# Optimization experiments

Measured on AMD Instinct MI355X. Metric: run time of the kernel, lower is better.

Reference implementation:

```python
import jax, jax.numpy as jnp
import numpy as np


def setup_inputs() -> dict:
    key = jax.random.key(0)
    k1, k2, k3, k4 = jax.random.split(key, 4)
    B, T, F_in, F_out, N, E, K = 16, 64, 64, 64, 128, 2, 4
    x = jax.random.normal(k1, (B, T, F_in, N), dtype=jnp.float32)
    # graph shift operator per (batch, time, edge-feature); scaled to keep powers bounded
    S = jax.random.normal(k2, (B, T, E, N, N), dtype=jnp.float32) / np.sqrt(N)
    H = jax.random.normal(k3, (F_out, E, K, F_in), dtype=jnp.float32) * 0.02
    bias = jax.random.normal(k4, (F_out, 1), dtype=jnp.float32) * 0.02
    return {"x": x, "S": S, "H": H, "bias": bias}


def reference(x, S, H, bias):
    # x: [B,T,F_in,N], S: [B,T,E,N,N], H: [F_out,E,K,F_in], bias: [F_out,1]
    B, T, F_in, N = x.shape
    E = S.shape[2]
    F_out, _, K, _ = H.shape
    # replicate features across edge-feature dim: [B,T,E,F_in,N]
    cur = jnp.broadcast_to(x[:, :, None], (B, T, E, F_in, N))
    taps = [cur]
    zero_row = jnp.zeros((B, 1, E, F_in, N), dtype=x.dtype)
    for _ in range(1, K):
        # time-shift: tap k at time t depends on tap k-1 at time t-1
        cur = jnp.concatenate([zero_row, cur[:, :-1]], axis=1)
        # diffuse over graph: [..,F_in,N] @ [..,N,N]
        cur = jnp.matmul(cur, S)
        taps.append(cur)
    z = jnp.stack(taps, axis=2)  # [B,T,K,E,F_in,N]
    # [B,T,N, E*K*F_in], matching permute(0,1,5,3,2,4) in the source
    z = z.transpose(0, 1, 5, 3, 2, 4).reshape(B, T, N, E * K * F_in)
    Hm = H.reshape(F_out, E * K * F_in)
    y = jnp.einsum('btnf,of->bton', z, Hm)  # [B,T,F_out,N]
    return y + bias  # bias [F_out,1] broadcasts over N
```

## Files before the change

kernel.cpp:

```cpp
#include <hip/hip_runtime.h>


namespace {
constexpr int B = 16, T = 64, F = 64, N = 128, E = 2, K = 4;
constexpr int SSW = 136;
constexpr int SZW = 136;
constexpr int TC = 8;
}

typedef short v8s __attribute__((ext_vector_type(8)));
typedef float v4f __attribute__((ext_vector_type(4)));

__device__ inline ushort f2bf(float f) {
  union { float f; uint u; } v; v.f = f;
  uint u = v.u;
  return (ushort)((u + 0x7fffu + ((u >> 16) & 1u)) >> 16);
}

__device__ inline uint pk2(float a, float b) {
  return (uint)f2bf(a) | ((uint)f2bf(b) << 16);
}

__device__ inline void tr64x128(const float* __restrict__ src,
                                ushort* __restrict__ dst, int dstride,
                                ushort* sh, int tid) {
  float4 r0[4], r1[4];
  #pragma unroll
  for (int it = 0; it < 4; ++it) {
    const int idx = tid + it * 256;
    const int m = idx >> 4, g = idx & 15;
    r0[it] = *(const float4*)(src + m * N + g * 8);
    r1[it] = *(const float4*)(src + m * N + g * 8 + 4);
  }
  #pragma unroll
  for (int it = 0; it < 4; ++it) {
    const int idx = tid + it * 256;
    const int m = idx >> 4, g = idx & 15;
    uint4 wv;
    wv.x = pk2(r0[it].x, r0[it].y); wv.y = pk2(r0[it].z, r0[it].w);
    wv.z = pk2(r1[it].x, r1[it].y); wv.w = pk2(r1[it].z, r1[it].w);
    *(uint4*)&sh[m * SSW + ((g ^ (m >> 3)) * 8)] = wv;
  }
  __syncthreads();
  const int bb = tid & 7, a = (tid >> 3) & 15, hh = tid >> 7;
  v8s rows[8];
  #pragma unroll
  for (int j = 0; j < 8; ++j)
    rows[j] = *(const v8s*)&sh[(8 * bb + j) * SSW + ((a ^ bb) * 8)];
  #pragma unroll
  for (int i = 0; i < 4; ++i) {
    const int e = 4 * hh + i;
    const int n = 8 * a + e;
    uint4 wv;
    wv.x = (uint)(ushort)rows[0][e] | ((uint)(ushort)rows[1][e] << 16);
    wv.y = (uint)(ushort)rows[2][e] | ((uint)(ushort)rows[3][e] << 16);
    wv.z = (uint)(ushort)rows[4][e] | ((uint)(ushort)rows[5][e] << 16);
    wv.w = (uint)(ushort)rows[6][e] | ((uint)(ushort)rows[7][e] << 16);
    *(uint4*)(dst + n * dstride + 8 * bb) = wv;
  }
}

__global__ __launch_bounds__(256) void gf_prep(
    const float* __restrict__ x, const float* __restrict__ H,
    ushort* __restrict__ xT, ushort* __restrict__ Hb) {
  __shared__ ushort sh[64 * SSW];
  const int bid = blockIdx.x;
  const int tid = threadIdx.x;
  if (bid < B * T) {
    tr64x128(x + (size_t)bid * F * N, xT + (size_t)bid * N * F, F, sh, tid);
  } else {
    const int hb = bid - B * T;
    const int d = (hb * 256 + tid) * 4;
    const int f = d & 63, o = (d >> 6) & 63, k = (d >> 12) & 3, e = (d >> 14) & 1;
    const float4 v = *(const float4*)(H + (((size_t)o * E + e) * K + k) * F + f);
    uint2 wv;
    wv.x = pk2(v.x, v.y);
    wv.y = pk2(v.z, v.w);
    *(uint2*)(Hb + d) = wv;
  }
}

__global__ __launch_bounds__(256, 2) void gf_fused(
    const float* __restrict__ S, const ushort* __restrict__ xT,
    const ushort* __restrict__ Hb, const float* __restrict__ bias,
    float* __restrict__ y) {
  __shared__ ushort sS[128 * SSW];
  __shared__ ushort sSt[6][16 * SZW];
  const int g = blockIdx.x;
  const int xcd = g & 7, loc = g >> 3;
  const int os = loc & 3, unitL = loc >> 2;
  const int unit = xcd * 16 + unitL;
  const int b = unit >> 3, chunk = unit & 7;
  const int t0 = chunk * TC;
  const int ob = os * 16;
  const int tid = threadIdx.x, w = tid >> 6, lane = tid & 63;
  const int l15 = lane & 15, q = lane >> 4;

  for (int i = tid; i < 6 * 16 * SZW; i += 256) ((ushort*)sSt)[i] = 0;

  v4f Yac[2];
  Yac[0][0] = 0.f; Yac[0][1] = 0.f; Yac[0][2] = 0.f; Yac[0][3] = 0.f;
  Yac[1] = Yac[0];

  const int tstart = (t0 == 0) ? 0 : t0 - 3;
  const int tS0 = (t0 == 0) ? 0 : t0 - 2;

  float4 pf0[8], pf1[8];
  {
    const float* Sg = S + (size_t)((b * T + tS0) * E + 0) * (N * N);
    #pragma unroll
    for (int j = 0; j < 8; ++j) {
      const int idx = tid + j * 256;
      const int m = idx >> 4, g2 = idx & 15;
      pf0[j] = *(const float4*)(Sg + m * N + g2 * 8);
      pf1[j] = *(const float4*)(Sg + m * N + g2 * 8 + 4);
    }
  }
  __syncthreads();

  for (int t = tstart; t < t0 + TC; ++t) {
    const bool staged = (t >= tS0);
    const bool emit = (t >= t0);
    for (int e = 0; e < E; ++e) {
      if (staged) {
        #pragma unroll
        for (int j = 0; j < 8; ++j) {
          const int idx = tid + j * 256;
          const int m = idx >> 4, g2 = idx & 15;
          uint4 wv;
          wv.x = pk2(pf0[j].x, pf0[j].y); wv.y = pk2(pf0[j].z, pf0[j].w);
          wv.z = pk2(pf1[j].x, pf1[j].y); wv.w = pk2(pf1[j].z, pf1[j].w);
          *(uint4*)&sS[m * SSW + ((g2 ^ (m >> 3)) * 8)] = wv;
        }
        const int nt = (e == 0) ? t : t + 1;
        const int ne = (e == 0) ? 1 : 0;
        if (nt < t0 + TC) {
          const float* Sg = S + (size_t)((b * T + nt) * E + ne) * (N * N);
          #pragma unroll
          for (int j = 0; j < 8; ++j) {
            const int idx = tid + j * 256;
            const int m = idx >> 4, g2 = idx & 15;
            pf0[j] = *(const float4*)(Sg + m * N + g2 * 8);
            pf1[j] = *(const float4*)(Sg + m * N + g2 * 8 + 4);
          }
        }
      }

      v4f Pn[2], Qn[2], U3n[2];
      #pragma unroll
      for (int mt = 0; mt < 2; ++mt) {
        Pn[mt][0] = 0.f; Pn[mt][1] = 0.f; Pn[mt][2] = 0.f; Pn[mt][3] = 0.f;
        Qn[mt] = Pn[mt]; U3n[mt] = Pn[mt];
      }
      {
        const ushort* xrow = xT + (size_t)(b * T + t) * (N * F);
        v8s xf[2][2];
        #pragma unroll
        for (int mt = 0; mt < 2; ++mt)
          #pragma unroll
          for (int fk = 0; fk < 2; ++fk)
            xf[mt][fk] = *(const v8s*)(xrow + ((2 * w + mt) * 16 + l15) * F +
                                       fk * 32 + q * 8);
        #pragma unroll
        for (int k = 0; k < 4; ++k) {
          if (k == 0 && !emit) continue;
          const ushort* hrow = Hb + ((size_t)((e * K + k) * 64) + ob + l15) * 64;
          v8s hf[2];
          hf[0] = *(const v8s*)(hrow + q * 8);
          hf[1] = *(const v8s*)(hrow + 32 + q * 8);
          v4f* tgt = (k == 0) ? Yac : (k == 1 ? Pn : (k == 2 ? Qn : U3n));
          #pragma unroll
          for (int fk = 0; fk < 2; ++fk)
            #pragma unroll
            for (int mt = 0; mt < 2; ++mt)
              tgt[mt] = __builtin_amdgcn_mfma_f32_16x16x32_bf16(
                  xf[mt][fk], hf[fk], tgt[mt], 0, 0, 0);
        }
      }

      if (staged) {
        __syncthreads();
        const int a2 = tid & 15, bg = tid >> 4;
        v8s rows[8];
        #pragma unroll
        for (int j = 0; j < 8; ++j)
          rows[j] = *(const v8s*)&sS[(8 * a2 + j) * SSW + ((bg ^ a2) * 8)];
        __syncthreads();
        #pragma unroll
        for (int i = 0; i < 8; ++i) {
          uint4 wv;
          wv.x = (uint)(ushort)rows[0][i] | ((uint)(ushort)rows[1][i] << 16);
          wv.y = (uint)(ushort)rows[2][i] | ((uint)(ushort)rows[3][i] << 16);
          wv.z = (uint)(ushort)rows[4][i] | ((uint)(ushort)rows[5][i] << 16);
          wv.w = (uint)(ushort)rows[6][i] | ((uint)(ushort)rows[7][i] << 16);
          *(uint4*)&sS[(8 * bg + i) * SSW + ((a2 ^ bg) * 8)] = wv;
        }
        __syncthreads();
        __builtin_amdgcn_s_setprio(1);
        #pragma unroll
        for (int c = 0; c < 4; ++c) {
          const int p = ((4 * c + q) + 2 * l15) & 15;
          const int sbase = l15 * SZW + p * 8;
          const v8s bzP = *(const v8s*)&sSt[e * 3 + 0][sbase];
          const v8s bzQ = *(const v8s*)&sSt[e * 3 + 1][sbase];
          const v8s bzU = *(const v8s*)&sSt[e * 3 + 2][sbase];
          #pragma unroll
          for (int mt = 0; mt < 2; ++mt) {
            const int n = (2 * w + mt) * 16 + l15;
            const v8s af = *(const v8s*)&sS[n * SSW +
                                            ((((c << 2) | q) ^ (n >> 3)) * 8)];
            if (emit)
              Yac[mt] = __builtin_amdgcn_mfma_f32_16x16x32_bf16(
                  af, bzP, Yac[mt], 0, 0, 0);
            Pn[mt] = __builtin_amdgcn_mfma_f32_16x16x32_bf16(
                af, bzQ, Pn[mt], 0, 0, 0);
            Qn[mt] = __builtin_amdgcn_mfma_f32_16x16x32_bf16(
                af, bzU, Qn[mt], 0, 0, 0);
          }
        }
        __builtin_amdgcn_s_setprio(0);
      }

      __syncthreads();
      #pragma unroll
      for (int mt = 0; mt < 2; ++mt) {
        const int cc = (2 * w + mt) * 2 + (q >> 1), h = q & 1;
        const int p = (cc + 2 * l15) & 15;
        const int base = l15 * SZW + p * 8 + h * 4;
        uint2 wv;
        wv.x = pk2(Pn[mt][0], Pn[mt][1]); wv.y = pk2(Pn[mt][2], Pn[mt][3]);
        *(uint2*)&sSt[e * 3 + 0][base] = wv;
        wv.x = pk2(Qn[mt][0], Qn[mt][1]); wv.y = pk2(Qn[mt][2], Qn[mt][3]);
        *(uint2*)&sSt[e * 3 + 1][base] = wv;
        wv.x = pk2(U3n[mt][0], U3n[mt][1]); wv.y = pk2(U3n[mt][2], U3n[mt][3]);
        *(uint2*)&sSt[e * 3 + 2][base] = wv;
      }

      if (e == 1 && emit) {
        float* yg = y + (size_t)(b * T + t) * (F * N);
        const float bv = bias[ob + l15];
        #pragma unroll
        for (int mt = 0; mt < 2; ++mt) {
          float4 v;
          v.x = Yac[mt][0] + bv; v.y = Yac[mt][1] + bv;
          v.z = Yac[mt][2] + bv; v.w = Yac[mt][3] + bv;
          *(float4*)(yg + (ob + l15) * N + (2 * w + mt) * 16 + q * 4) = v;
          Yac[mt][0] = 0.f; Yac[mt][1] = 0.f;
          Yac[mt][2] = 0.f; Yac[mt][3] = 0.f;
        }
      }
    }
  }
}

extern "C" void kernel_launch(void* const* d_in, const int* in_sizes, int n_in,
                              void* d_out, int out_size, void* d_ws, size_t ws_size,
                              hipStream_t stream) {
  const float* x    = (const float*)d_in[0];
  const float* S    = (const float*)d_in[1];
  const float* H    = (const float*)d_in[2];
  const float* bias = (const float*)d_in[3];
  float* y = (float*)d_out;

  const size_t XTn = (size_t)B * T * N * F;
  ushort* xT = (ushort*)d_ws;
  ushort* Hb = xT + XTn;

  gf_prep <<<B * T + 32, 256, 0, stream>>>(x, H, xT, Hb);
  gf_fused<<<512,        256, 0, stream>>>(S, xT, Hb, bias, y);
}
```

Measured before the change: 294.5 us.

## Stage S transposed directly from registers and prefetch next x tile

The S prefetch is reorganised so each wave loads column pairs across 32 rows and writes the bf16 S transpose straight into shared memory. This removes the in-LDS transpose pass and its three barriers. The x fragments for the next time step are now prefetched a step ahead, and __syncthreads is replaced by a custom barrier that waits only on LDS counters. In exchange, per-thread register use rises (32 float2 for S plus doubled x fragments), and the narrower float2 global loads may coalesce less efficiently.

```diff
diff --git a/kernel.cpp b/kernel.cpp
--- a/kernel.cpp
+++ b/kernel.cpp
@@ -20,6 +20,12 @@
 __device__ inline uint pk2(float a, float b) {
   return (uint)f2bf(a) | ((uint)f2bf(b) << 16);
 }
+
+#define LBAR() do { \
+  asm volatile("s_waitcnt lgkmcnt(0)" ::: "memory"); \
+  __builtin_amdgcn_s_barrier(); \
+  __builtin_amdgcn_sched_barrier(0); \
+} while (0)
 
 __device__ inline void tr64x128(const float* __restrict__ src,
                                 ushort* __restrict__ dst, int dstride,
@@ -84,8 +90,8 @@
     const float* __restrict__ S, const ushort* __restrict__ xT,
     const ushort* __restrict__ Hb, const float* __restrict__ bias,
     float* __restrict__ y) {
-  __shared__ ushort sS[128 * SSW];
-  __shared__ ushort sSt[6][16 * SZW];
+  __shared__ __align__(16) ushort sST[128 * SSW];
+  __shared__ __align__(16) ushort sSt[6][16 * SZW];
   const int g = blockIdx.x;
   const int xcd = g & 7, loc = g >> 3;
   const int os = loc & 3, unitL = loc >> 2;
@@ -105,46 +111,69 @@
   const int tstart = (t0 == 0) ? 0 : t0 - 3;
   const int tS0 = (t0 == 0) ? 0 : t0 - 2;
 
-  float4 pf0[8], pf1[8];
+  float2 pfS[32];
   {
-    const float* Sg = S + (size_t)((b * T + tS0) * E + 0) * (N * N);
-    #pragma unroll
-    for (int j = 0; j < 8; ++j) {
-      const int idx = tid + j * 256;
-      const int m = idx >> 4, g2 = idx & 15;
-      pf0[j] = *(const float4*)(Sg + m * N + g2 * 8);
-      pf1[j] = *(const float4*)(Sg + m * N + g2 * 8 + 4);
-    }
-  }
-  __syncthreads();
+    const float* Sg = S + (size_t)((b * T + tS0) * E + 0) * (N * N) +
+                      (size_t)(32 * w) * N + 2 * lane;
+    #pragma unroll
+    for (int j = 0; j < 32; ++j) pfS[j] = *(const float2*)(Sg + j * N);
+  }
+  v8s xfc[2][2], xfn[2][2];
+  {
+    const ushort* xrow = xT + (size_t)(b * T + tstart) * (N * F);
+    #pragma unroll
+    for (int mt = 0; mt < 2; ++mt)
+      #pragma unroll
+      for (int fk = 0; fk < 2; ++fk)
+        xfc[mt][fk] = *(const v8s*)(xrow + ((2 * w + mt) * 16 + l15) * F +
+                                    fk * 32 + q * 8);
+  }
+
+  LBAR();
 
   for (int t = tstart; t < t0 + TC; ++t) {
     const bool staged = (t >= tS0);
     const bool emit = (t >= t0);
+
+    {
+      const int tn = (t + 1 < t0 + TC) ? t + 1 : t;
+      const ushort* xrow = xT + (size_t)(b * T + tn) * (N * F);
+      #pragma unroll
+      for (int mt = 0; mt < 2; ++mt)
+        #pragma unroll
+        for (int fk = 0; fk < 2; ++fk)
+          xfn[mt][fk] = *(const v8s*)(xrow + ((2 * w + mt) * 16 + l15) * F +
+                                      fk * 32 + q * 8);
+    }
+
+    #pragma unroll
     for (int e = 0; e < E; ++e) {
       if (staged) {
         #pragma unroll
-        for (int j = 0; j < 8; ++j) {
-          const int idx = tid + j * 256;
-          const int m = idx >> 4, g2 = idx & 15;
-          uint4 wv;
-          wv.x = pk2(pf0[j].x, pf0[j].y); wv.y = pk2(pf0[j].z, pf0[j].w);
-          wv.z = pk2(pf1[j].x, pf1[j].y); wv.w = pk2(pf1[j].z, pf1[j].w);
-          *(uint4*)&sS[m * SSW + ((g2 ^ (m >> 3)) * 8)] = wv;
+        for (int r = 0; r < 2; ++r) {
+          const int n = 2 * lane + r;
+          const int nb = n >> 3;
+          #pragma unroll
+          for (int i = 0; i < 4; ++i) {
+            const float2* p0 = &pfS[8 * i];
+            uint4 wv;
+            wv.x = r ? pk2(p0[0].y, p0[1].y) : pk2(p0[0].x, p0[1].x);
+            wv.y = r ? pk2(p0[2].y, p0[3].y) : pk2(p0[2].x, p0[3].x);
+            wv.z = r ? pk2(p0[4].y, p0[5].y) : pk2(p0[4].x, p0[5].x);
+            wv.w = r ? pk2(p0[6].y, p0[7].y) : pk2(p0[6].x, p0[7].x);
+            *(uint4*)&sST[n * SSW + (((4 * w + i) ^ nb) * 8)] = wv;
+          }
         }
         const int nt = (e == 0) ? t : t + 1;
-        const int ne = (e == 0) ? 1 : 0;
+        const int ne = e ^ 1;
         if (nt < t0 + TC) {
-          const float* Sg = S + (size_t)((b * T + nt) * E + ne) * (N * N);
-          #pragma unroll
-          for (int j = 0; j < 8; ++j) {
-            const int idx = tid + j * 256;
-            const int m = idx >> 4, g2 = idx & 15;
-            pf0[j] = *(const float4*)(Sg + m * N + g2 * 8);
-            pf1[j] = *(const float4*)(Sg + m * N + g2 * 8 + 4);
-          }
-        }
-      }
+          const float* Sg = S + (size_t)((b * T + nt) * E + ne) * (N * N) +
+                            (size_t)(32 * w) * N + 2 * lane;
+          #pragma unroll
+          for (int j = 0; j < 32; ++j) pfS[j] = *(const float2*)(Sg + j * N);
+        }
+      }
+      LBAR();
 
       v4f Pn[2], Qn[2], U3n[2];
       #pragma unroll
@@ -152,50 +181,23 @@
         Pn[mt][0] = 0.f; Pn[mt][1] = 0.f; Pn[mt][2] = 0.f; Pn[mt][3] = 0.f;
         Qn[mt] = Pn[mt]; U3n[mt] = Pn[mt];
       }
-      {
-        const ushort* xrow = xT + (size_t)(b * T + t) * (N * F);
-        v8s xf[2][2];
-        #pragma unroll
-        for (int mt = 0; mt < 2; ++mt)
-          #pragma unroll
-          for (int fk = 0; fk < 2; ++fk)
-            xf[mt][fk] = *(const v8s*)(xrow + ((2 * w + mt) * 16 + l15) * F +
-                                       fk * 32 + q * 8);
-        #pragma unroll
-        for (int k = 0; k < 4; ++k) {
-          if (k == 0 && !emit) continue;
-          const ushort* hrow = Hb + ((size_t)((e * K + k) * 64) + ob + l15) * 64;
-          v8s hf[2];
-          hf[0] = *(const v8s*)(hrow + q * 8);
-          hf[1] = *(const v8s*)(hrow + 32 + q * 8);
-          v4f* tgt = (k == 0) ? Yac : (k == 1 ? Pn : (k == 2 ? Qn : U3n));
-          #pragma unroll
-          for (int fk = 0; fk < 2; ++fk)
-            #pragma unroll
-            for (int mt = 0; mt < 2; ++mt)
-              tgt[mt] = __builtin_amdgcn_mfma_f32_16x16x32_bf16(
-                  xf[mt][fk], hf[fk], tgt[mt], 0, 0, 0);
-        }
+      #pragma unroll
+      for (int k = 0; k < 4; ++k) {
+        if (k == 0 && !emit) continue;
+        const ushort* hrow = Hb + ((size_t)((e * K + k) * 64) + ob + l15) * 64;
+        v8s hf[2];
+        hf[0] = *(const v8s*)(hrow + q * 8);
+        hf[1] = *(const v8s*)(hrow + 32 + q * 8);
+        v4f* tgt = (k == 0) ? Yac : (k == 1 ? Pn : (k == 2 ? Qn : U3n));
+        #pragma unroll
+        for (int fk = 0; fk < 2; ++fk)
+          #pragma unroll
+          for (int mt = 0; mt < 2; ++mt)
+            tgt[mt] = __builtin_amdgcn_mfma_f32_16x16x32_bf16(
+                xfc[mt][fk], hf[fk], tgt[mt], 0, 0, 0);
       }
 
       if (staged) {
-        __syncthreads();
-        const int a2 = tid & 15, bg = tid >> 4;
-        v8s rows[8];
-        #pragma unroll
-        for (int j = 0; j < 8; ++j)
-          rows[j] = *(const v8s*)&sS[(8 * a2 + j) * SSW + ((bg ^ a2) * 8)];
-        __syncthreads();
-        #pragma unroll
-        for (int i = 0; i < 8; ++i) {
-          uint4 wv;
-          wv.x = (uint)(ushort)rows[0][i] | ((uint)(ushort)rows[1][i] << 16);
-          wv.y = (uint)(ushort)rows[2][i] | ((uint)(ushort)rows[3][i] << 16);
-          wv.z = (uint)(ushort)rows[4][i] | ((uint)(ushort)rows[5][i] << 16);
-          wv.w = (uint)(ushort)rows[6][i] | ((uint)(ushort)rows[7][i] << 16);
-          *(uint4*)&sS[(8 * bg + i) * SSW + ((a2 ^ bg) * 8)] = wv;
-        }
-        __syncthreads();
         __builtin_amdgcn_s_setprio(1);
         #pragma unroll
         for (int c = 0; c < 4; ++c) {
@@ -207,8 +209,8 @@
           #pragma unroll
           for (int mt = 0; mt < 2; ++mt) {
             const int n = (2 * w + mt) * 16 + l15;
-            const v8s af = *(const v8s*)&sS[n * SSW +
-                                            ((((c << 2) | q) ^ (n >> 3)) * 8)];
+            const v8s af = *(const v8s*)&sST[n * SSW +
+                                             ((((c << 2) | q) ^ (n >> 3)) * 8)];
             if (emit)
               Yac[mt] = __builtin_amdgcn_mfma_f32_16x16x32_bf16(
                   af, bzP, Yac[mt], 0, 0, 0);
@@ -220,8 +222,8 @@
         }
         __builtin_amdgcn_s_setprio(0);
       }
-
-      __syncthreads();
+      LBAR();
+
       #pragma unroll
       for (int mt = 0; mt < 2; ++mt) {
         const int cc = (2 * w + mt) * 2 + (q >> 1), h = q & 1;
@@ -250,6 +252,12 @@
         }
       }
     }
+
+    #pragma unroll
+    for (int mt = 0; mt < 2; ++mt)
+      #pragma unroll
+      for (int fk = 0; fk < 2; ++fk)
+        xfc[mt][fk] = xfn[mt][fk];
   }
 }
 
```

New measurement: 305.0 us. +3.6%, slower.
